# Optimization experiments

Measured on AMD Instinct MI355X. Metric: run time of the kernel, lower is better.

Reference implementation:

```python
import jax, jax.numpy as jnp
import numpy as np

EPS_BN = 1e-5   # torch BatchNorm1d default eps
EPS_D = 1e-8    # pointops interpolation eps
K = 3           # pointops.nearestneighbor returns 3 nearest neighbors

B, N1, N2 = 4, 8192, 2048
IN_PLANES, OUT_PLANES = 512, 256


def setup_inputs() -> dict:
    key = jax.random.key(0)
    ks = jax.random.split(key, 8)
    return {
        "p1": jax.random.normal(ks[0], (B, N1, 3), jnp.float32),
        "x1": jax.random.normal(ks[1], (B, N1, OUT_PLANES), jnp.float32),
        "p2": jax.random.normal(ks[2], (B, N2, 3), jnp.float32),
        "x2": jax.random.normal(ks[3], (B, N2, IN_PLANES), jnp.float32),
        # linear1: Linear(out_planes, out_planes) + BN + ReLU (acts on x1)
        "W1": jax.random.normal(ks[4], (OUT_PLANES, OUT_PLANES), jnp.float32) / np.sqrt(OUT_PLANES),
        "b1": jax.random.normal(ks[5], (OUT_PLANES,), jnp.float32) * 0.01,
        "gamma1": jnp.ones((OUT_PLANES,), jnp.float32),
        "beta1": jnp.zeros((OUT_PLANES,), jnp.float32),
        # linear2: Linear(in_planes, out_planes) + BN + ReLU (acts on x2)
        "W2": jax.random.normal(ks[6], (IN_PLANES, OUT_PLANES), jnp.float32) / np.sqrt(IN_PLANES),
        "b2": jax.random.normal(ks[7], (OUT_PLANES,), jnp.float32) * 0.01,
        "gamma2": jnp.ones((OUT_PLANES,), jnp.float32),
        "beta2": jnp.zeros((OUT_PLANES,), jnp.float32),
    }


def _bn(x, gamma, beta):
    # BatchNorm1d_P: normalize each channel over (batch, points) with batch stats
    m = jnp.mean(x, axis=(0, 1))
    v = jnp.var(x, axis=(0, 1))
    return (x - m) * jax.lax.rsqrt(v + EPS_BN) * gamma + beta


def reference(p1, x1, p2, x2, W1, b1, gamma1, beta1, W2, b2, gamma2, beta2):
    # linear2 on coarse features: [B,N2,in] -> [B,N2,out]
    h2 = jax.nn.relu(_bn(x2 @ W2 + b2, gamma2, beta2))
    # 3-NN of each p1 point among p2 points, squared distances [B,N1,N2]
    d = (jnp.sum(p1 * p1, -1)[:, :, None]
         + jnp.sum(p2 * p2, -1)[:, None, :]
         - 2.0 * jnp.einsum('bnd,bmd->bnm', p1, p2))
    neg_d, idx = jax.lax.top_k(-d, K)          # [B,N1,K]
    dist = -neg_d
    dist_recip = 1.0 / (dist + EPS_D)
    weight = dist_recip / jnp.sum(dist_recip, -1, keepdims=True)  # [B,N1,K]
    gathered = jax.vmap(lambda f, i: f[i])(h2, idx)               # [B,N1,K,out]
    interp = jnp.einsum('bnk,bnkc->bnc', weight, gathered)        # [B,N1,out]
    # linear1 on fine features: [B,N1,out] -> [B,N1,out]
    h1 = jax.nn.relu(_bn(x1 @ W1 + b1, gamma1, beta1))
    return interp + h1
```

## Files before the change

kernel.cpp:

```cpp
#include <hip/hip_runtime.h>

#define B_   4
#define N1_  8192
#define N2_  2048
#define CIN  512
#define COUT 256

typedef __attribute__((ext_vector_type(8))) short bf16x8;
typedef __attribute__((ext_vector_type(4))) float f32x4;

__device__ inline short f2bf(float f) {
  union { float f; unsigned u; } v; v.f = f;
  unsigned r = v.u + 0x7fffu + ((v.u >> 16) & 1u);
  return (short)(r >> 16);
}
__device__ inline float bf2f(short s) {
  union { unsigned u; float f; } v; v.u = ((unsigned)(unsigned short)s) << 16;
  return v.f;
}
__device__ inline float relu_(float x) { return fmaxf(x, 0.0f); }

#define INS(d, j)                                                   \
  { bool lt0 = (d) < d0, lt1 = (d) < d1, lt2 = (d) < d2;            \
    d2 = lt1 ? d1 : (lt2 ? (d) : d2); i2 = lt1 ? i1 : (lt2 ? (j) : i2); \
    d1 = lt0 ? d0 : (lt1 ? (d) : d1); i1 = lt0 ? i0 : (lt1 ? (j) : i1); \
    d0 = lt0 ? (d) : d0;              i0 = lt0 ? (j) : i0; }

__global__ __launch_bounds__(256) void knn_prep(
    const float* __restrict__ p1, const float* __restrict__ p2,
    const float* __restrict__ W1, const float* __restrict__ W2,
    float* __restrict__ wgt, int* __restrict__ idx,
    short* __restrict__ Wt1, short* __restrict__ Wt2,
    float* __restrict__ stats)
{
  __shared__ float4 sp2[N2_];
  const int bid = blockIdx.x;
  const int tid = threadIdx.x;

  if (bid >= 1024) {
    const int w = bid - 1024;
    if (w < 256) {
      int k = w * 256 + tid;
      Wt1[(size_t)(k & 255) * COUT + (k >> 8)] = f2bf(W1[k]);
    } else if (w < 768) {
      int k = (w - 256) * 256 + tid;
      Wt2[(size_t)(k & 255) * CIN + (k >> 8)] = f2bf(W2[k]);
    } else {
      stats[(w - 768) * 256 + tid] = 0.0f;
    }
    return;
  }

  const int b = bid & 3;
  const int qg = bid >> 2;
  const float* P2 = p2 + (size_t)b * N2_ * 3;
  for (int j = tid; j < N2_; j += 256) {
    float x = P2[j * 3 + 0], y = P2[j * 3 + 1], z = P2[j * 3 + 2];
    sp2[j] = make_float4(x, y, z, x * x + y * y + z * z);
  }
  __syncthreads();

  const int sub = tid & 7;
  const int q = qg * 32 + (tid >> 3);
  const float* P1 = p1 + ((size_t)b * N1_ + q) * 3;
  const float x = P1[0], y = P1[1], z = P1[2];
  const float s1 = x * x + y * y + z * z;
  const float nx = -2.0f * x, ny = -2.0f * y, nz = -2.0f * z;

  float d0 = 1e30f, d1 = 1e30f, d2 = 1e30f;
  int i0 = 0, i1 = 0, i2 = 0;
  const float4* base = &sp2[sub];
  int jb = sub;
  for (int t = 0; t < 32; t++) {
    #pragma unroll
    for (int u = 0; u < 8; u++) {
      float4 qq = base[u * 8];
      float d = fmaf(nx, qq.x, fmaf(ny, qq.y, fmaf(nz, qq.z, qq.w)));
      INS(d, jb + u * 8);
    }
    base += 64;
    jb += 64;
  }

  #pragma unroll
  for (int m = 1; m < 8; m <<= 1) {
    float e0 = __shfl_xor(d0, m), e1 = __shfl_xor(d1, m), e2 = __shfl_xor(d2, m);
    int j0 = __shfl_xor(i0, m), j1 = __shfl_xor(i1, m), j2 = __shfl_xor(i2, m);
    INS(e0, j0); INS(e1, j1); INS(e2, j2);
  }

  if (sub == 0) {
    float r0 = 1.0f / (d0 + s1 + 1e-8f);
    float r1 = 1.0f / (d1 + s1 + 1e-8f);
    float r2 = 1.0f / (d2 + s1 + 1e-8f);
    float rs = 1.0f / (r0 + r1 + r2);
    size_t o = ((size_t)b * N1_ + q) * 3;
    wgt[o + 0] = r0 * rs; wgt[o + 1] = r1 * rs; wgt[o + 2] = r2 * rs;
    idx[o + 0] = i0;      idx[o + 1] = i1;      idx[o + 2] = i2;
  }
}

#define BM 64
#define BN 128
#define BK 64

__global__ __launch_bounds__(256) void gemm_fused(
    const float* __restrict__ x1, const float* __restrict__ x2,
    const short* __restrict__ Wt1, const short* __restrict__ Wt2,
    const float* __restrict__ bias1, const float* __restrict__ bias2,
    short* __restrict__ y1, short* __restrict__ y2,
    float* __restrict__ stats)
{
  __shared__ __align__(16) short As[BM][BK + 8];
  __shared__ __align__(16) short Bs[BN][BK + 8];

  const int bid = blockIdx.x;
  const float* X; const short* Wt; const float* bias; short* Y; float* st;
  int K, mb, nb;
  if (bid < 256) {
    X = x2; Wt = Wt2; bias = bias2; Y = y2; st = stats + 512; K = CIN;
    mb = bid >> 1; nb = bid & 1;
  } else {
    const int t = bid - 256;
    X = x1; Wt = Wt1; bias = bias1; Y = y1; st = stats; K = COUT;
    mb = t >> 1; nb = t & 1;
  }
  const int bm = mb * BM;
  const int bn = nb * BN;

  const int tid = threadIdx.x;
  const int lane = tid & 63;
  const int wave = tid >> 6;
  const int wm = (wave & 1) * 32;
  const int wn = (wave >> 1) * 64;

  f32x4 acc[2][4];
  for (int i = 0; i < 2; i++)
    for (int j = 0; j < 4; j++)
      for (int e = 0; e < 4; e++) acc[i][j][e] = 0.0f;

  const int ar = tid >> 4;
  const int ak = (tid & 15) * 4;
  const int br = tid >> 3;
  const int bk = (tid & 7) * 8;

  for (int k0 = 0; k0 < K; k0 += BK) {
    #pragma unroll
    for (int r = ar; r < BM; r += 16) {
      float4 v = *(const float4*)&X[(size_t)(bm + r) * K + k0 + ak];
      short4 s = { f2bf(v.x), f2bf(v.y), f2bf(v.z), f2bf(v.w) };
      *(short4*)&As[r][ak] = s;
    }
    #pragma unroll
    for (int r = br; r < BN; r += 32) {
      *(bf16x8*)&Bs[r][bk] = *(const bf16x8*)&Wt[(size_t)(bn + r) * K + k0 + bk];
    }
    __syncthreads();

    const int fr = lane & 15;
    const int kq = (lane >> 4) * 8;
    #pragma unroll
    for (int ks = 0; ks < BK; ks += 32) {
      bf16x8 a0 = *(const bf16x8*)&As[wm + fr][ks + kq];
      bf16x8 a1 = *(const bf16x8*)&As[wm + 16 + fr][ks + kq];
      bf16x8 b0 = *(const bf16x8*)&Bs[wn + fr][ks + kq];
      bf16x8 b1 = *(const bf16x8*)&Bs[wn + 16 + fr][ks + kq];
      bf16x8 b2 = *(const bf16x8*)&Bs[wn + 32 + fr][ks + kq];
      bf16x8 b3 = *(const bf16x8*)&Bs[wn + 48 + fr][ks + kq];
      acc[0][0] = __builtin_amdgcn_mfma_f32_16x16x32_bf16(a0, b0, acc[0][0], 0, 0, 0);
      acc[0][1] = __builtin_amdgcn_mfma_f32_16x16x32_bf16(a0, b1, acc[0][1], 0, 0, 0);
      acc[0][2] = __builtin_amdgcn_mfma_f32_16x16x32_bf16(a0, b2, acc[0][2], 0, 0, 0);
      acc[0][3] = __builtin_amdgcn_mfma_f32_16x16x32_bf16(a0, b3, acc[0][3], 0, 0, 0);
      acc[1][0] = __builtin_amdgcn_mfma_f32_16x16x32_bf16(a1, b0, acc[1][0], 0, 0, 0);
      acc[1][1] = __builtin_amdgcn_mfma_f32_16x16x32_bf16(a1, b1, acc[1][1], 0, 0, 0);
      acc[1][2] = __builtin_amdgcn_mfma_f32_16x16x32_bf16(a1, b2, acc[1][2], 0, 0, 0);
      acc[1][3] = __builtin_amdgcn_mfma_f32_16x16x32_bf16(a1, b3, acc[1][3], 0, 0, 0);
    }
    __syncthreads();
  }

  const int col = lane & 15;
  const int rq = (lane >> 4) * 4;
  float cs[4], cs2[4];
  #pragma unroll
  for (int ni = 0; ni < 4; ni++) { cs[ni] = 0.0f; cs2[ni] = 0.0f; }

  #pragma unroll
  for (int mi = 0; mi < 2; mi++) {
    #pragma unroll
    for (int ni = 0; ni < 4; ni++) {
      const int gm = bm + wm + mi * 16 + rq;
      const int gn = bn + wn + ni * 16 + col;
      const float bb = bias[gn];
      #pragma unroll
      for (int j = 0; j < 4; j++) {
        float v = acc[mi][ni][j] + bb;
        Y[(size_t)(gm + j) * 256 + gn] = f2bf(v);
        cs[ni] += v;
        cs2[ni] += v * v;
      }
    }
  }
  #pragma unroll
  for (int ni = 0; ni < 4; ni++) {
    cs[ni]  += __shfl_xor(cs[ni], 16);  cs[ni]  += __shfl_xor(cs[ni], 32);
    cs2[ni] += __shfl_xor(cs2[ni], 16); cs2[ni] += __shfl_xor(cs2[ni], 32);
  }
  if (lane < 16) {
    #pragma unroll
    for (int ni = 0; ni < 4; ni++) {
      const int gn = bn + wn + ni * 16 + col;
      atomicAdd(&st[gn], cs[ni]);
      atomicAdd(&st[256 + gn], cs2[ni]);
    }
  }
}

__global__ __launch_bounds__(256) void final_out(
    const short* __restrict__ y1, const short* __restrict__ y2,
    const float* __restrict__ stats,
    const float* __restrict__ gamma1, const float* __restrict__ beta1,
    const float* __restrict__ gamma2, const float* __restrict__ beta2,
    const float* __restrict__ wgt, const int* __restrict__ idx,
    float* __restrict__ out)
{
  const int r = blockIdx.x * 4 + (threadIdx.x >> 6);
  const int lane = threadIdx.x & 63;
  const int b = r >> 13;
  const int c = lane * 4;

  const float invM1 = 1.0f / (B_ * N1_), invM2 = 1.0f / (B_ * N2_);
  float4 su1 = *(const float4*)&stats[c];
  float4 sq1 = *(const float4*)&stats[256 + c];
  float4 su2 = *(const float4*)&stats[512 + c];
  float4 sq2 = *(const float4*)&stats[768 + c];
  float4 gm1 = *(const float4*)&gamma1[c];
  float4 bt1 = *(const float4*)&beta1[c];
  float4 gm2 = *(const float4*)&gamma2[c];
  float4 bt2 = *(const float4*)&beta2[c];

  float4 sc1, sh1, sc2, sh2;
  {
    float m, v;
    m = su1.x * invM1; v = sq1.x * invM1 - m * m; sc1.x = gm1.x * rsqrtf(v + 1e-5f); sh1.x = bt1.x - m * sc1.x;
    m = su1.y * invM1; v = sq1.y * invM1 - m * m; sc1.y = gm1.y * rsqrtf(v + 1e-5f); sh1.y = bt1.y - m * sc1.y;
    m = su1.z * invM1; v = sq1.z * invM1 - m * m; sc1.z = gm1.z * rsqrtf(v + 1e-5f); sh1.z = bt1.z - m * sc1.z;
    m = su1.w * invM1; v = sq1.w * invM1 - m * m; sc1.w = gm1.w * rsqrtf(v + 1e-5f); sh1.w = bt1.w - m * sc1.w;
    m = su2.x * invM2; v = sq2.x * invM2 - m * m; sc2.x = gm2.x * rsqrtf(v + 1e-5f); sh2.x = bt2.x - m * sc2.x;
    m = su2.y * invM2; v = sq2.y * invM2 - m * m; sc2.y = gm2.y * rsqrtf(v + 1e-5f); sh2.y = bt2.y - m * sc2.y;
    m = su2.z * invM2; v = sq2.z * invM2 - m * m; sc2.z = gm2.z * rsqrtf(v + 1e-5f); sh2.z = bt2.z - m * sc2.z;
    m = su2.w * invM2; v = sq2.w * invM2 - m * m; sc2.w = gm2.w * rsqrtf(v + 1e-5f); sh2.w = bt2.w - m * sc2.w;
  }

  const size_t wo = (size_t)r * 3;
  const float w0 = wgt[wo], w1 = wgt[wo + 1], w2 = wgt[wo + 2];
  const int i0 = idx[wo], i1 = idx[wo + 1], i2 = idx[wo + 2];

  const short* g0 = y2 + ((size_t)b * N2_ + i0) * 256;
  const short* g1 = y2 + ((size_t)b * N2_ + i1) * 256;
  const short* g2 = y2 + ((size_t)b * N2_ + i2) * 256;

  short4 s0 = *(const short4*)&g0[c];
  short4 s1 = *(const short4*)&g1[c];
  short4 s2 = *(const short4*)&g2[c];
  short4 sv = *(const short4*)&y1[(size_t)r * 256 + c];

  float4 o;
  o.x = w0 * relu_(bf2f(s0.x) * sc2.x + sh2.x) + w1 * relu_(bf2f(s1.x) * sc2.x + sh2.x)
      + w2 * relu_(bf2f(s2.x) * sc2.x + sh2.x) + relu_(bf2f(sv.x) * sc1.x + sh1.x);
  o.y = w0 * relu_(bf2f(s0.y) * sc2.y + sh2.y) + w1 * relu_(bf2f(s1.y) * sc2.y + sh2.y)
      + w2 * relu_(bf2f(s2.y) * sc2.y + sh2.y) + relu_(bf2f(sv.y) * sc1.y + sh1.y);
  o.z = w0 * relu_(bf2f(s0.z) * sc2.z + sh2.z) + w1 * relu_(bf2f(s1.z) * sc2.z + sh2.z)
      + w2 * relu_(bf2f(s2.z) * sc2.z + sh2.z) + relu_(bf2f(sv.z) * sc1.z + sh1.z);
  o.w = w0 * relu_(bf2f(s0.w) * sc2.w + sh2.w) + w1 * relu_(bf2f(s1.w) * sc2.w + sh2.w)
      + w2 * relu_(bf2f(s2.w) * sc2.w + sh2.w) + relu_(bf2f(sv.w) * sc1.w + sh1.w);

  *(float4*)&out[(size_t)r * 256 + c] = o;
}

extern "C" void kernel_launch(void* const* d_in, const int* in_sizes, int n_in,
                              void* d_out, int out_size, void* d_ws, size_t ws_size,
                              hipStream_t stream)
{
  const float* p1  = (const float*)d_in[0];
  const float* x1  = (const float*)d_in[1];
  const float* p2  = (const float*)d_in[2];
  const float* x2  = (const float*)d_in[3];
  const float* W1  = (const float*)d_in[4];
  const float* b1  = (const float*)d_in[5];
  const float* g1  = (const float*)d_in[6];
  const float* be1 = (const float*)d_in[7];
  const float* W2  = (const float*)d_in[8];
  const float* b2  = (const float*)d_in[9];
  const float* g2  = (const float*)d_in[10];
  const float* be2 = (const float*)d_in[11];
  float* out = (float*)d_out;
  char* ws = (char*)d_ws;

  short* y1    = (short*)(ws + 0);
  short* y2    = (short*)(ws + 16777216);
  short* Wt1   = (short*)(ws + 20971520);
  short* Wt2   = (short*)(ws + 21102592);
  float* stats = (float*)(ws + 21364736);
  float* wgt   = (float*)(ws + 21368832);
  int*   idx   = (int*)  (ws + 21762048);

  knn_prep<<<1796, 256, 0, stream>>>(p1, p2, W1, W2, wgt, idx, Wt1, Wt2, stats);

  gemm_fused<<<1280, 256, 0, stream>>>(x1, x2, Wt1, Wt2, b1, b2, y1, y2, stats);

  final_out<<<(B_ * N1_) / 4, 256, 0, stream>>>(
      y1, y2, stats, g1, be1, g2, be2, wgt, idx, out);
}
```

Measured before the change: 202.2 us.

## Pre-convert activations to bf16, use 128x128 GEMM tiles with direct global-to-LDS loads

```diff
diff --git a/kernel.cpp b/kernel.cpp
--- a/kernel.cpp
+++ b/kernel.cpp
@@ -1,4 +1,5 @@
 #include <hip/hip_runtime.h>
+#include <stdint.h>
 
 #define B_   4
 #define N1_  8192
@@ -20,33 +21,58 @@
 }
 __device__ inline float relu_(float x) { return fmaxf(x, 0.0f); }
 
-#define INS(d, j)                                                   \
-  { bool lt0 = (d) < d0, lt1 = (d) < d1, lt2 = (d) < d2;            \
-    d2 = lt1 ? d1 : (lt2 ? (d) : d2); i2 = lt1 ? i1 : (lt2 ? (j) : i2); \
-    d1 = lt0 ? d0 : (lt1 ? (d) : d1); i1 = lt0 ? i0 : (lt1 ? (j) : i1); \
+typedef const __attribute__((address_space(1))) unsigned int* gas_t;
+typedef __attribute__((address_space(3))) unsigned int* las_t;
+__device__ __forceinline__ void g2l16(const short* g, short* l) {
+  __builtin_amdgcn_global_load_lds((gas_t)g, (las_t)l, 16, 0, 0);
+}
+
+#define KNN_B  512
+#define W1_B0  512
+#define W2_B0  768
+#define ST_B0  1280
+#define CV1_B0 1284
+#define CV2_B0 9476
+#define TOT_B  13572
+
+#define INS3(d, j, d0, d1, d2, i0, i1, i2)                                \
+  { bool lt0 = (d) < d0, lt1 = (d) < d1, lt2 = (d) < d2;                  \
+    d2 = lt1 ? d1 : (lt2 ? (d) : d2); i2 = lt1 ? i1 : (lt2 ? (j) : i2);   \
+    d1 = lt0 ? d0 : (lt1 ? (d) : d1); i1 = lt0 ? i0 : (lt1 ? (j) : i1);   \
     d0 = lt0 ? (d) : d0;              i0 = lt0 ? (j) : i0; }
 
 __global__ __launch_bounds__(256) void knn_prep(
     const float* __restrict__ p1, const float* __restrict__ p2,
     const float* __restrict__ W1, const float* __restrict__ W2,
+    const float* __restrict__ x1, const float* __restrict__ x2,
     float* __restrict__ wgt, int* __restrict__ idx,
     short* __restrict__ Wt1, short* __restrict__ Wt2,
+    short* __restrict__ x1b, short* __restrict__ x2b,
     float* __restrict__ stats)
 {
   __shared__ float4 sp2[N2_];
   const int bid = blockIdx.x;
   const int tid = threadIdx.x;
 
-  if (bid >= 1024) {
-    const int w = bid - 1024;
-    if (w < 256) {
-      int k = w * 256 + tid;
-      Wt1[(size_t)(k & 255) * COUT + (k >> 8)] = f2bf(W1[k]);
-    } else if (w < 768) {
-      int k = (w - 256) * 256 + tid;
+  if (bid >= KNN_B) {
+    if (bid >= CV2_B0) {
+      int i = (bid - CV2_B0) * 256 + tid;
+      float4 v = ((const float4*)x2)[i];
+      short4 s = { f2bf(v.x), f2bf(v.y), f2bf(v.z), f2bf(v.w) };
+      ((short4*)x2b)[i] = s;
+    } else if (bid >= CV1_B0) {
+      int i = (bid - CV1_B0) * 256 + tid;
+      float4 v = ((const float4*)x1)[i];
+      short4 s = { f2bf(v.x), f2bf(v.y), f2bf(v.z), f2bf(v.w) };
+      ((short4*)x1b)[i] = s;
+    } else if (bid >= ST_B0) {
+      stats[(bid - ST_B0) * 256 + tid] = 0.0f;
+    } else if (bid >= W2_B0) {
+      int k = (bid - W2_B0) * 256 + tid;
       Wt2[(size_t)(k & 255) * CIN + (k >> 8)] = f2bf(W2[k]);
     } else {
-      stats[(w - 768) * 256 + tid] = 0.0f;
+      int k = (bid - W1_B0) * 256 + tid;
+      Wt1[(size_t)(k & 255) * COUT + (k >> 8)] = f2bf(W1[k]);
     }
     return;
   }
@@ -61,22 +87,30 @@
   __syncthreads();
 
   const int sub = tid & 7;
-  const int q = qg * 32 + (tid >> 3);
-  const float* P1 = p1 + ((size_t)b * N1_ + q) * 3;
-  const float x = P1[0], y = P1[1], z = P1[2];
-  const float s1 = x * x + y * y + z * z;
-  const float nx = -2.0f * x, ny = -2.0f * y, nz = -2.0f * z;
-
-  float d0 = 1e30f, d1 = 1e30f, d2 = 1e30f;
-  int i0 = 0, i1 = 0, i2 = 0;
+  const int q0 = qg * 64 + (tid >> 3);
+  const int q1 = q0 + 32;
+  const float* A0 = p1 + ((size_t)b * N1_ + q0) * 3;
+  const float* A1 = p1 + ((size_t)b * N1_ + q1) * 3;
+  const float ax = A0[0], ay = A0[1], az = A0[2];
+  const float bx = A1[0], by = A1[1], bz = A1[2];
+  const float sA = ax * ax + ay * ay + az * az;
+  const float sB = bx * bx + by * by + bz * bz;
+  const float nax = -2.0f * ax, nay = -2.0f * ay, naz = -2.0f * az;
+  const float nbx = -2.0f * bx, nby = -2.0f * by, nbz = -2.0f * bz;
+
+  float a0 = 1e30f, a1 = 1e30f, a2 = 1e30f; int ia0 = 0, ia1 = 0, ia2 = 0;
+  float b0 = 1e30f, b1 = 1e30f, b2 = 1e30f; int ib0 = 0, ib1 = 0, ib2 = 0;
+
   const float4* base = &sp2[sub];
   int jb = sub;
   for (int t = 0; t < 32; t++) {
     #pragma unroll
     for (int u = 0; u < 8; u++) {
       float4 qq = base[u * 8];
-      float d = fmaf(nx, qq.x, fmaf(ny, qq.y, fmaf(nz, qq.z, qq.w)));
-      INS(d, jb + u * 8);
+      float dA = fmaf(nax, qq.x, fmaf(nay, qq.y, fmaf(naz, qq.z, qq.w)));
+      float dB = fmaf(nbx, qq.x, fmaf(nby, qq.y, fmaf(nbz, qq.z, qq.w)));
+      INS3(dA, jb + u * 8, a0, a1, a2, ia0, ia1, ia2);
+      INS3(dB, jb + u * 8, b0, b1, b2, ib0, ib1, ib2);
     }
     base += 64;
     jb += 64;
@@ -84,109 +118,122 @@
 
   #pragma unroll
   for (int m = 1; m < 8; m <<= 1) {
-    float e0 = __shfl_xor(d0, m), e1 = __shfl_xor(d1, m), e2 = __shfl_xor(d2, m);
-    int j0 = __shfl_xor(i0, m), j1 = __shfl_xor(i1, m), j2 = __shfl_xor(i2, m);
-    INS(e0, j0); INS(e1, j1); INS(e2, j2);
+    float e0 = __shfl_xor(a0, m), e1 = __shfl_xor(a1, m), e2 = __shfl_xor(a2, m);
+    int j0 = __shfl_xor(ia0, m), j1 = __shfl_xor(ia1, m), j2 = __shfl_xor(ia2, m);
+    INS3(e0, j0, a0, a1, a2, ia0, ia1, ia2);
+    INS3(e1, j1, a0, a1, a2, ia0, ia1, ia2);
+    INS3(e2, j2, a0, a1, a2, ia0, ia1, ia2);
+    float f0 = __shfl_xor(b0, m), f1 = __shfl_xor(b1, m), f2 = __shfl_xor(b2, m);
+    int k0 = __shfl_xor(ib0, m), k1 = __shfl_xor(ib1, m), k2 = __shfl_xor(ib2, m);
+    INS3(f0, k0, b0, b1, b2, ib0, ib1, ib2);
+    INS3(f1, k1, b0, b1, b2, ib0, ib1, ib2);
+    INS3(f2, k2, b0, b1, b2, ib0, ib1, ib2);
   }
 
   if (sub == 0) {
-    float r0 = 1.0f / (d0 + s1 + 1e-8f);
-    float r1 = 1.0f / (d1 + s1 + 1e-8f);
-    float r2 = 1.0f / (d2 + s1 + 1e-8f);
-    float rs = 1.0f / (r0 + r1 + r2);
-    size_t o = ((size_t)b * N1_ + q) * 3;
-    wgt[o + 0] = r0 * rs; wgt[o + 1] = r1 * rs; wgt[o + 2] = r2 * rs;
-    idx[o + 0] = i0;      idx[o + 1] = i1;      idx[o + 2] = i2;
-  }
-}
-
-#define BM 64
-#define BN 128
-#define BK 64
+    {
+      float r0 = 1.0f / (a0 + sA + 1e-8f);
+      float r1 = 1.0f / (a1 + sA + 1e-8f);
+      float r2 = 1.0f / (a2 + sA + 1e-8f);
+      float rs = 1.0f / (r0 + r1 + r2);
+      size_t o = ((size_t)b * N1_ + q0) * 3;
+      wgt[o + 0] = r0 * rs; wgt[o + 1] = r1 * rs; wgt[o + 2] = r2 * rs;
+      idx[o + 0] = ia0;     idx[o + 1] = ia1;     idx[o + 2] = ia2;
+    }
+    {
+      float r0 = 1.0f / (b0 + sB + 1e-8f);
+      float r1 = 1.0f / (b1 + sB + 1e-8f);
+      float r2 = 1.0f / (b2 + sB + 1e-8f);
+      float rs = 1.0f / (r0 + r1 + r2);
+      size_t o = ((size_t)b * N1_ + q1) * 3;
+      wgt[o + 0] = r0 * rs; wgt[o + 1] = r1 * rs; wgt[o + 2] = r2 * rs;
+      idx[o + 0] = ib0;     idx[o + 1] = ib1;     idx[o + 2] = ib2;
+    }
+  }
+}
+
+#define GBM 128
+#define GBN 128
+#define GBK 64
 
 __global__ __launch_bounds__(256) void gemm_fused(
-    const float* __restrict__ x1, const float* __restrict__ x2,
+    const short* __restrict__ x1b, const short* __restrict__ x2b,
     const short* __restrict__ Wt1, const short* __restrict__ Wt2,
     const float* __restrict__ bias1, const float* __restrict__ bias2,
     short* __restrict__ y1, short* __restrict__ y2,
     float* __restrict__ stats)
 {
-  __shared__ __align__(16) short As[BM][BK + 8];
-  __shared__ __align__(16) short Bs[BN][BK + 8];
+  __shared__ __align__(16) short As[GBM * GBK];
+  __shared__ __align__(16) short Bs[GBN * GBK];
 
   const int bid = blockIdx.x;
-  const float* X; const short* Wt; const float* bias; short* Y; float* st;
+  const short* X; const short* Wt; const float* bias; short* Y; float* st;
   int K, mb, nb;
-  if (bid < 256) {
-    X = x2; Wt = Wt2; bias = bias2; Y = y2; st = stats + 512; K = CIN;
+  if (bid < 128) {
+    X = x2b; Wt = Wt2; bias = bias2; Y = y2; st = stats + 512; K = CIN;
     mb = bid >> 1; nb = bid & 1;
   } else {
-    const int t = bid - 256;
-    X = x1; Wt = Wt1; bias = bias1; Y = y1; st = stats; K = COUT;
+    const int t = bid - 128;
+    X = x1b; Wt = Wt1; bias = bias1; Y = y1; st = stats; K = COUT;
     mb = t >> 1; nb = t & 1;
   }
-  const int bm = mb * BM;
-  const int bn = nb * BN;
-
-  const int tid = threadIdx.x;
-  const int lane = tid & 63;
-  const int wave = tid >> 6;
-  const int wm = (wave & 1) * 32;
-  const int wn = (wave >> 1) * 64;
-
-  f32x4 acc[2][4];
-  for (int i = 0; i < 2; i++)
+  const int bm = mb * GBM;
+  const int bn = nb * GBN;
+
+  const int tid = threadIdx.x, lane = tid & 63, wave = tid >> 6;
+  const int wm = (wave & 1) * 64, wn = (wave >> 1) * 64;
+
+  f32x4 acc[4][4];
+  #pragma unroll
+  for (int i = 0; i < 4; i++)
+    #pragma unroll
     for (int j = 0; j < 4; j++)
+      #pragma unroll
       for (int e = 0; e < 4; e++) acc[i][j][e] = 0.0f;
 
-  const int ar = tid >> 4;
-  const int ak = (tid & 15) * 4;
-  const int br = tid >> 3;
-  const int bk = (tid & 7) * 8;
-
-  for (int k0 = 0; k0 < K; k0 += BK) {
-    #pragma unroll
-    for (int r = ar; r < BM; r += 16) {
-      float4 v = *(const float4*)&X[(size_t)(bm + r) * K + k0 + ak];
-      short4 s = { f2bf(v.x), f2bf(v.y), f2bf(v.z), f2bf(v.w) };
-      *(short4*)&As[r][ak] = s;
-    }
-    #pragma unroll
-    for (int r = br; r < BN; r += 32) {
-      *(bf16x8*)&Bs[r][bk] = *(const bf16x8*)&Wt[(size_t)(bn + r) * K + k0 + bk];
+  const int lr = lane >> 3;
+  const int lp = (lane & 7) ^ lr;
+  const int lk = lp * 8;
+
+  const int fr = lane & 15;
+  const int quad = lane >> 4;
+  const int pA0 = ((quad ^ (fr & 7)) * 16);
+
+  for (int k0 = 0; k0 < K; k0 += GBK) {
+    #pragma unroll
+    for (int i = 0; i < 4; i++) {
+      const int crow = wave * 4 + i;
+      g2l16(X  + (size_t)(bm + crow * 8 + lr) * K + k0 + lk, As + crow * 512);
+      g2l16(Wt + (size_t)(bn + crow * 8 + lr) * K + k0 + lk, Bs + crow * 512);
     }
     __syncthreads();
 
-    const int fr = lane & 15;
-    const int kq = (lane >> 4) * 8;
-    #pragma unroll
-    for (int ks = 0; ks < BK; ks += 32) {
-      bf16x8 a0 = *(const bf16x8*)&As[wm + fr][ks + kq];
-      bf16x8 a1 = *(const bf16x8*)&As[wm + 16 + fr][ks + kq];
-      bf16x8 b0 = *(const bf16x8*)&Bs[wn + fr][ks + kq];
-      bf16x8 b1 = *(const bf16x8*)&Bs[wn + 16 + fr][ks + kq];
-      bf16x8 b2 = *(const bf16x8*)&Bs[wn + 32 + fr][ks + kq];
-      bf16x8 b3 = *(const bf16x8*)&Bs[wn + 48 + fr][ks + kq];
-      acc[0][0] = __builtin_amdgcn_mfma_f32_16x16x32_bf16(a0, b0, acc[0][0], 0, 0, 0);
-      acc[0][1] = __builtin_amdgcn_mfma_f32_16x16x32_bf16(a0, b1, acc[0][1], 0, 0, 0);
-      acc[0][2] = __builtin_amdgcn_mfma_f32_16x16x32_bf16(a0, b2, acc[0][2], 0, 0, 0);
-      acc[0][3] = __builtin_amdgcn_mfma_f32_16x16x32_bf16(a0, b3, acc[0][3], 0, 0, 0);
-      acc[1][0] = __builtin_amdgcn_mfma_f32_16x16x32_bf16(a1, b0, acc[1][0], 0, 0, 0);
-      acc[1][1] = __builtin_amdgcn_mfma_f32_16x16x32_bf16(a1, b1, acc[1][1], 0, 0, 0);
-      acc[1][2] = __builtin_amdgcn_mfma_f32_16x16x32_bf16(a1, b2, acc[1][2], 0, 0, 0);
-      acc[1][3] = __builtin_amdgcn_mfma_f32_16x16x32_bf16(a1, b3, acc[1][3], 0, 0, 0);
+    #pragma unroll
+    for (int ks = 0; ks < 2; ks++) {
+      const int xo = ks * 64;
+      bf16x8 af[4], bf[4];
+      #pragma unroll
+      for (int i = 0; i < 4; i++) {
+        af[i] = *(const bf16x8*)((const char*)As + (wm + i * 16 + fr) * 128 + (pA0 ^ xo));
+        bf[i] = *(const bf16x8*)((const char*)Bs + (wn + i * 16 + fr) * 128 + (pA0 ^ xo));
+      }
+      #pragma unroll
+      for (int i = 0; i < 4; i++)
+        #pragma unroll
+        for (int j = 0; j < 4; j++)
+          acc[i][j] = __builtin_amdgcn_mfma_f32_16x16x32_bf16(af[i], bf[j], acc[i][j], 0, 0, 0);
     }
     __syncthreads();
   }
 
-  const int col = lane & 15;
-  const int rq = (lane >> 4) * 4;
+  const int col = fr;
+  const int rq = quad * 4;
   float cs[4], cs2[4];
   #pragma unroll
   for (int ni = 0; ni < 4; ni++) { cs[ni] = 0.0f; cs2[ni] = 0.0f; }
 
   #pragma unroll
-  for (int mi = 0; mi < 2; mi++) {
+  for (int mi = 0; mi < 4; mi++) {
     #pragma unroll
     for (int ni = 0; ni < 4; ni++) {
       const int gm = bm + wm + mi * 16 + rq;
@@ -299,15 +346,18 @@
 
   short* y1    = (short*)(ws + 0);
   short* y2    = (short*)(ws + 16777216);
-  short* Wt1   = (short*)(ws + 20971520);
-  short* Wt2   = (short*)(ws + 21102592);
-  float* stats = (float*)(ws + 21364736);
-  float* wgt   = (float*)(ws + 21368832);
-  int*   idx   = (int*)  (ws + 21762048);
-
-  knn_prep<<<1796, 256, 0, stream>>>(p1, p2, W1, W2, wgt, idx, Wt1, Wt2, stats);
-
-  gemm_fused<<<1280, 256, 0, stream>>>(x1, x2, Wt1, Wt2, b1, b2, y1, y2, stats);
+  short* x1b   = (short*)(ws + 20971520);
+  short* x2b   = (short*)(ws + 37748736);
+  short* Wt1   = (short*)(ws + 46137344);
+  short* Wt2   = (short*)(ws + 46268416);
+  float* stats = (float*)(ws + 46530560);
+  float* wgt   = (float*)(ws + 46534656);
+  int*   idx   = (int*)  (ws + 46927872);
+
+  knn_prep<<<TOT_B, 256, 0, stream>>>(p1, p2, W1, W2, x1, x2,
+                                      wgt, idx, Wt1, Wt2, x1b, x2b, stats);
+
+  gemm_fused<<<640, 256, 0, stream>>>(x1b, x2b, Wt1, Wt2, b1, b2, y1, y2, stats);
 
   final_out<<<(B_ * N1_) / 4, 256, 0, stream>>>(
       y1, y2, stats, g1, be1, g2, be2, wgt, idx, out);
```

New measurement: 177.1 us. -12.4%, faster.
